# Optimization experiments

Hardware: AMD Instinct MI355X
Metric: run time of the kernel (lower is better)

The kernel has to match this reference:

```python
import jax, jax.numpy as jnp
import numpy as np

N_NODES = 100000
N_EDGES = 1600000
F_IN = 64
HID = 64
N_CLASSES = 45
N_GRAPHS = 256


def gcn_conv(x, src, dst, W, b, n):
    # GCNConv with added self-loops and symmetric normalization (PyG semantics)
    h = x @ W  # [N, H]
    deg = jax.ops.segment_sum(jnp.ones(src.shape[0], h.dtype), dst, num_segments=n) + 1.0
    dinv = jax.lax.rsqrt(deg)  # deg^{-1/2}, deg >= 1 due to self loops
    coef = dinv[src] * dinv[dst]  # [E]
    msg = h[src] * coef[:, None]  # gather + scale
    agg = jax.ops.segment_sum(msg, dst, num_segments=n)  # scatter-add to dst
    agg = agg + h * (dinv * dinv)[:, None]  # self-loop contribution
    return agg + b


def setup_inputs() -> dict:
    key = jax.random.key(0)
    ks = jax.random.split(key, 12)
    x = jax.random.normal(ks[0], (N_NODES, F_IN), dtype=jnp.float32)
    edge_index = jax.random.randint(ks[1], (2, N_EDGES), 0, N_NODES, dtype=jnp.int32)
    batch = jnp.sort(jax.random.randint(ks[2], (N_NODES,), 0, N_GRAPHS, dtype=jnp.int32))
    s1 = 1.0 / np.sqrt(F_IN)
    s2 = 1.0 / np.sqrt(HID)
    W1 = jax.random.uniform(ks[3], (F_IN, HID), jnp.float32, -s1, s1)
    b1 = jnp.zeros((HID,), jnp.float32)
    W2 = jax.random.uniform(ks[4], (HID, HID), jnp.float32, -s2, s2)
    b2 = jnp.zeros((HID,), jnp.float32)
    W3 = jax.random.uniform(ks[5], (HID, HID), jnp.float32, -s2, s2)
    b3 = jnp.zeros((HID,), jnp.float32)
    Wl = jax.random.uniform(ks[6], (HID, N_CLASSES), jnp.float32, -s2, s2)
    bl = jnp.zeros((N_CLASSES,), jnp.float32)
    return {"x": x, "edge_index": edge_index, "batch": batch,
            "W1": W1, "b1": b1, "W2": W2, "b2": b2, "W3": W3, "b3": b3,
            "Wl": Wl, "bl": bl}


def reference(x, edge_index, batch, W1, b1, W2, b2, W3, b3, Wl, bl):
    n = x.shape[0]
    src, dst = edge_index[0], edge_index[1]
    h = jax.nn.relu(gcn_conv(x, src, dst, W1, b1, n))
    h = jax.nn.relu(gcn_conv(h, src, dst, W2, b2, n))
    h = gcn_conv(h, src, dst, W3, b3, n)
    # global mean pool over graph segments
    sums = jax.ops.segment_sum(h, batch, num_segments=N_GRAPHS)  # [G, H]
    cnts = jax.ops.segment_sum(jnp.ones(n, h.dtype), batch, num_segments=N_GRAPHS)
    pooled = sums / jnp.maximum(cnts, 1.0)[:, None]
    # dropout is identity in eval mode
    return pooled @ Wl + bl  # [G, num_classes]
```

## Files before the change

kernel.cpp:

```cpp
#include <hip/hip_runtime.h>
#include <hip/hip_bf16.h>

#define N_NODES   100000
#define N_EDGES   1600000
#define F_IN      64
#define HID       64
#define N_CLASSES 45
#define N_GRAPHS  256
#define SB        392
#define NPB       256
#define CAP       4608
#define WPB       72
#define CHUNK     4096
#define NCHUNK    391
#define NZB       192
#define GEMM_GRID 3125
#define AGGE_GRID 7056
#define NZB2      192
#define ZLEN4_F   1600000
#define ZLEN4_A   1604096

__device__ __forceinline__ float rl_f(float v, int k) {
    return __uint_as_float(__builtin_amdgcn_readlane(__float_as_uint(v), k));
}
__device__ __forceinline__ int rl_i(int v, int k) {
    return __builtin_amdgcn_readlane(v, k);
}
__device__ __forceinline__ unsigned short f2bf(float x) {
    unsigned u = __float_as_uint(x);
    unsigned r = u + 0x7FFFu + ((u >> 16) & 1u);
    return (unsigned short)(r >> 16);
}
__device__ __forceinline__ float bf2f(unsigned short h) {
    return __uint_as_float(((unsigned)h) << 16);
}
__device__ __forceinline__ unsigned scale2(unsigned u, float dv) {
    float lo = __uint_as_float(u << 16) * dv;
    float hi = __uint_as_float(u & 0xFFFF0000u) * dv;
    return (((unsigned)f2bf(hi)) << 16) | (unsigned)f2bf(lo);
}

__global__ __launch_bounds__(256) void k_front(const int* __restrict__ src, const int* __restrict__ dst,
                                               int* __restrict__ bcur, int* __restrict__ binned,
                                               const float* __restrict__ x, const float* __restrict__ W1,
                                               unsigned short* __restrict__ P, float* __restrict__ zbase) {
    int bid = blockIdx.x;
    int t   = threadIdx.x;
    if (bid < NCHUNK) {
        __shared__ int stg[CHUNK];
        __shared__ unsigned short bkt[CHUNK];
        __shared__ int h[512], cur[512], off[512];
        __shared__ int ps[256];
        h[t] = 0; h[t + 256] = 0;
        __syncthreads();
        int base4 = bid * (CHUNK / 4);
        #pragma unroll
        for (int i = 0; i < CHUNK / 1024; i++) {
            int e4 = base4 + i * 256 + t;
            if (e4 < N_EDGES / 4) {
                int4 d = ((const int4*)dst)[e4];
                atomicAdd(&h[d.x >> 8], 1);
                atomicAdd(&h[d.y >> 8], 1);
                atomicAdd(&h[d.z >> 8], 1);
                atomicAdd(&h[d.w >> 8], 1);
            }
        }
        __syncthreads();
        int a0 = h[2 * t], a1 = h[2 * t + 1];
        ps[t] = a0 + a1;
        __syncthreads();
        for (int o = 1; o < 256; o <<= 1) {
            int v = (t >= o) ? ps[t - o] : 0;
            __syncthreads();
            if (t >= o) ps[t] += v;
            __syncthreads();
        }
        int pex = ps[t] - (a0 + a1);
        int e0 = pex, e1 = pex + a0;
        cur[2 * t] = e0; cur[2 * t + 1] = e1;
        if (2 * t < SB && a0 > 0)
            off[2 * t] = (2 * t) * CAP + atomicAdd(&bcur[2 * t], a0) - e0;
        if (2 * t + 1 < SB && a1 > 0)
            off[2 * t + 1] = (2 * t + 1) * CAP + atomicAdd(&bcur[2 * t + 1], a1) - e1;
        __syncthreads();
        int total = ps[255];
        #pragma unroll
        for (int i = 0; i < CHUNK / 1024; i++) {
            int e4 = base4 + i * 256 + t;
            if (e4 < N_EDGES / 4) {
                int4 d  = ((const int4*)dst)[e4];
                int4 s4 = ((const int4*)src)[e4];
                int q;
                q = atomicAdd(&cur[d.x >> 8], 1); stg[q] = s4.x | ((d.x & 255) << 17); bkt[q] = (unsigned short)(d.x >> 8);
                q = atomicAdd(&cur[d.y >> 8], 1); stg[q] = s4.y | ((d.y & 255) << 17); bkt[q] = (unsigned short)(d.y >> 8);
                q = atomicAdd(&cur[d.z >> 8], 1); stg[q] = s4.z | ((d.z & 255) << 17); bkt[q] = (unsigned short)(d.z >> 8);
                q = atomicAdd(&cur[d.w >> 8], 1); stg[q] = s4.w | ((d.w & 255) << 17); bkt[q] = (unsigned short)(d.w >> 8);
            }
        }
        __syncthreads();
        for (int i = t; i < total; i += 256) {
            int b = bkt[i];
            binned[off[b] + i] = stg[i];
        }
    } else if (bid < NCHUNK + NZB) {
        float4 z = make_float4(0.f, 0.f, 0.f, 0.f);
        float4* zp = (float4*)zbase;
        int zb = bid - NCHUNK;
        for (long i = (long)zb * 256 + t; i < (long)ZLEN4_F; i += (long)NZB * 256)
            zp[i] = z;
    } else {
        int gbid = bid - NCHUNK - NZB;
        int lane = t & 63;
        int wv   = t >> 6;
        int base = gbid * 32 + wv * 8;
        float xr[8], acc[8];
        #pragma unroll
        for (int r = 0; r < 8; r++) {
            xr[r]  = x[(size_t)(base + r) * 64 + lane];
            acc[r] = 0.f;
        }
        for (int kb = 0; kb < 64; kb += 8) {
            float wb[8];
            #pragma unroll
            for (int j = 0; j < 8; j++) wb[j] = W1[(kb + j) * 64 + lane];
            #pragma unroll
            for (int j = 0; j < 8; j++) {
                #pragma unroll
                for (int r = 0; r < 8; r++)
                    acc[r] = fmaf(rl_f(xr[r], kb + j), wb[j], acc[r]);
            }
        }
        #pragma unroll
        for (int r = 0; r < 8; r++)
            P[(size_t)(base + r) * 64 + lane] = f2bf(acc[r]);
    }
}

__global__ __launch_bounds__(1024) void k_bcsr(const int* __restrict__ binned, const int* __restrict__ bcur,
                                               float* __restrict__ dinv, float* __restrict__ dinv2,
                                               int* __restrict__ csr, unsigned short* __restrict__ P) {
    __shared__ int bin_s[CAP];
    __shared__ int cs_s[CAP];
    __shared__ int h[NPB];
    __shared__ int ts[NPB];
    __shared__ float sdv[NPB];
    int t = threadIdx.x;
    int b = blockIdx.x;
    int nb0  = b << 8;
    int ebeg = b * CAP;
    int ecnt = bcur[b]; if (ecnt > CAP) ecnt = CAP;
    if (t < NPB) h[t] = 0;
    __syncthreads();
    for (int i = t; i < ecnt; i += 1024) {
        int p = binned[ebeg + i];
        bin_s[i] = p;
        atomicAdd(&h[p >> 17], 1);
    }
    __syncthreads();
    int c = 0;
    if (t < NPB) { c = h[t]; ts[t] = c; }
    __syncthreads();
    for (int o = 1; o < NPB; o <<= 1) {
        int v = (t >= o && t < NPB) ? ts[t - o] : 0;
        __syncthreads();
        if (t >= o && t < NPB) ts[t] += v;
        __syncthreads();
    }
    if (t < NPB) {
        int n = nb0 + t;
        float dval = 0.f;
        if (n < N_NODES) {
            float inv = 1.0f / (float)(c + 1);
            dinv2[n] = inv;
            dval     = sqrtf(inv);
            dinv[n]  = dval;
        }
        sdv[t] = dval;
        h[t] = ts[t] - c;
    }
    __syncthreads();
    for (int i = t; i < ecnt; i += 1024) {
        int p = bin_s[i];
        int q = atomicAdd(&h[p >> 17], 1);
        cs_s[q] = p;
    }
    __syncthreads();
    for (int i = t; i < ecnt; i += 1024)
        csr[ebeg + i] = cs_s[i];
    for (int i = t; i < NPB * 8; i += 1024) {
        int row = i >> 3;
        int nn  = nb0 + row;
        if (nn >= N_NODES) break;
        float dv = sdv[row];
        uint4* pp = (uint4*)P + (size_t)nn * 8 + (i & 7);
        uint4 v = *pp;
        v.x = scale2(v.x, dv); v.y = scale2(v.y, dv);
        v.z = scale2(v.z, dv); v.w = scale2(v.w, dv);
        *pp = v;
    }
}

template<bool POOLI>
__global__ __launch_bounds__(256) void k_gemm(const float* __restrict__ E,
                                              unsigned short* P,
                                              const float* __restrict__ W,
                                              const float* __restrict__ bprev,
                                              const float* __restrict__ bcurr,
                                              const float* __restrict__ dinv,
                                              const float* __restrict__ dinv2,
                                              const int* __restrict__ batch,
                                              float* __restrict__ pool) {
    int lane = threadIdx.x & 63;
    int wv   = threadIdx.x >> 6;
    int base = blockIdx.x * 32 + wv * 8;
    float bp = bprev[lane];
    float xr[8], acc[8], dn[8];
    #pragma unroll
    for (int r = 0; r < 8; r++) dn[r] = dinv[base + r];
    #pragma unroll
    for (int r = 0; r < 8; r++) {
        int n = base + r;
        float hp = bf2f(P[(size_t)n * 64 + lane]);
        float a  = E[(size_t)n * 64 + lane] + fmaf(hp, dn[r], bp);
        xr[r]  = fmaxf(a, 0.f);
        acc[r] = 0.f;
    }
    for (int kb = 0; kb < 64; kb += 8) {
        float wb[8];
        #pragma unroll
        for (int j = 0; j < 8; j++) wb[j] = W[(kb + j) * 64 + lane];
        #pragma unroll
        for (int j = 0; j < 8; j++) {
            #pragma unroll
            for (int r = 0; r < 8; r++)
                acc[r] = fmaf(rl_f(xr[r], kb + j), wb[j], acc[r]);
        }
    }
    #pragma unroll
    for (int r = 0; r < 8; r++)
        P[(size_t)(base + r) * 64 + lane] = f2bf(acc[r] * dn[r]);
    if (POOLI) {
        float bv = bcurr[lane];
        float d2[8];
        #pragma unroll
        for (int r = 0; r < 8; r++) d2[r] = dinv2[base + r];
        int g0 = batch[base], g7 = batch[base + 7];
        if (g0 == g7) {
            float s = 0.f;
            #pragma unroll
            for (int r = 0; r < 8; r++) s += fmaf(acc[r], d2[r], bv);
            atomicAdd(&pool[g0 * 64 + lane], s);
        } else {
            #pragma unroll
            for (int r = 0; r < 8; r++) {
                int g = batch[base + r];
                atomicAdd(&pool[g * 64 + lane], fmaf(acc[r], d2[r], bv));
            }
        }
    }
}

template<bool POOLEP, bool ZROLE>
__global__ __launch_bounds__(256, 8) void k_agge(const unsigned short* __restrict__ Hbuf,
                                                 const int* __restrict__ csr,
                                                 const int* __restrict__ bcur,
                                                 const float* __restrict__ dinv,
                                                 const int* __restrict__ batch,
                                                 float* __restrict__ Out,
                                                 float* __restrict__ zbase) {
    int t = threadIdx.x;
    if (ZROLE && blockIdx.x >= AGGE_GRID) {
        float4 z = make_float4(0.f, 0.f, 0.f, 0.f);
        float4* zp = (float4*)zbase;
        int zb = blockIdx.x - AGGE_GRID;
        for (long i = (long)zb * 256 + t; i < (long)ZLEN4_A; i += (long)NZB2 * 256)
            zp[i] = z;
        return;
    }
    int wv   = t >> 6;
    int lane = t & 63;
    int wid  = blockIdx.x * 4 + wv;
    int b    = wid / WPB;
    int lw   = wid - b * WPB;
    int used = bcur[b]; if (used > CAP) used = CAP;
    int e0   = lw * 64;
    int rem  = used - e0;
    if (rem <= 0) return;
    if (rem > 64) rem = 64;
    int base = b * CAP + e0;

    int p = 0;
    if (lane < rem) p = csr[base + lane];
    int sv = p & 0x1FFFF;
    int dv = p >> 17;

    int dvp = __shfl_up(dv, 1);
    unsigned long long m0 = __ballot(dv != dvp);
    unsigned mlo = __builtin_amdgcn_readfirstlane((unsigned)m0);
    unsigned mhi = __builtin_amdgcn_readfirstlane((unsigned)(m0 >> 32));
    unsigned long long mask = ((((unsigned long long)mhi) << 32) | mlo) & ~1ull;

    auto flush1 = [&](int dl, float a) {
        int dst = (b << 8) + dl;
        if (dst < N_NODES) {
            float val = dinv[dst] * a;
            if (POOLEP) {
                int g = batch[dst];
                atomicAdd(&Out[g * 64 + lane], val);
            } else {
                atomicAdd(&Out[(size_t)dst * 64 + lane], val);
            }
        }
    };

    int cur = rl_i(dv, 0);
    float acc = 0.f;
    int j = 0;
    for (; j + 16 <= rem; j += 16) {
        unsigned short u[16];
        #pragma unroll
        for (int i = 0; i < 16; i++) {
            int s = rl_i(sv, j + i);
            u[i] = Hbuf[(size_t)s * 64 + lane];
        }
        #pragma unroll
        for (int i = 0; i < 16; i++) {
            if ((mask >> (j + i)) & 1) {
                flush1(cur, acc); acc = 0.f; cur = rl_i(dv, j + i);
            }
            acc += bf2f(u[i]);
        }
    }
    for (; j < rem; j++) {
        int s0 = rl_i(sv, j);
        unsigned short u0 = Hbuf[(size_t)s0 * 64 + lane];
        if ((mask >> j) & 1) { flush1(cur, acc); acc = 0.f; cur = rl_i(dv, j); }
        acc += bf2f(u0);
    }
    flush1(cur, acc);
}

__device__ __forceinline__ int lbound(const int* __restrict__ a, int n, int v) {
    int lo = 0, hi = n;
    while (lo < hi) { int m = (lo + hi) >> 1; if (a[m] < v) lo = m + 1; else hi = m; }
    return lo;
}

__global__ __launch_bounds__(64) void k_cls(const float* __restrict__ pool, const int* __restrict__ batch,
                                            const float* __restrict__ Wl, const float* __restrict__ bl,
                                            float* __restrict__ out) {
    __shared__ float pm[64];
    __shared__ int bounds[2];
    int g = blockIdx.x;
    int t = threadIdx.x;
    if (t < 2) bounds[t] = lbound(batch, N_NODES, g + t);
    __syncthreads();
    float cnt = (float)(bounds[1] - bounds[0]);
    pm[t] = pool[g * 64 + t] / fmaxf(cnt, 1.0f);
    __syncthreads();
    if (t < N_CLASSES) {
        float o = bl[t];
        #pragma unroll
        for (int k = 0; k < HID; k++) o = fmaf(pm[k], Wl[k * N_CLASSES + t], o);
        out[g * N_CLASSES + t] = o;
    }
}


extern "C" void kernel_launch(void* const* d_in, const int* in_sizes, int n_in,
                              void* d_out, int out_size, void* d_ws, size_t ws_size,
                              hipStream_t stream) {
    const float* x     = (const float*)d_in[0];
    const int*   eidx  = (const int*)  d_in[1];
    const int*   batch = (const int*)  d_in[2];
    const float* W1 = (const float*)d_in[3];
    const float* b1 = (const float*)d_in[4];
    const float* W2 = (const float*)d_in[5];
    const float* b2 = (const float*)d_in[6];
    const float* W3 = (const float*)d_in[7];
    const float* b3 = (const float*)d_in[8];
    const float* Wl = (const float*)d_in[9];
    const float* bl = (const float*)d_in[10];
    const int* src = eidx;
    const int* dst = eidx + N_EDGES;

    char* p = (char*)d_ws;
    auto alloc = [&](size_t bytes) -> void* {
        void* r = (void*)p;
        p += (bytes + 255) & ~(size_t)255;
        return r;
    };
    float* dinv  = (float*)alloc((size_t)N_NODES * 4);
    float* dinv2 = (float*)alloc((size_t)N_NODES * 4);
    int*   csr   = (int*)  alloc((size_t)SB * CAP * 4);
    unsigned short* P = (unsigned short*)alloc((size_t)N_NODES * 64 * 2);
    float* E1    = (float*)alloc((size_t)N_NODES * 64 * 4);
    float* pool  = (float*)alloc((size_t)N_GRAPHS * 64 * 4);
    float* E2    = (float*)alloc((size_t)N_NODES * 64 * 4);
    int*   bcur  = (int*)  alloc((size_t)SB * 4);
    int*   binned = (int*) alloc((size_t)SB * CAP * 4);

    const int front_grid = NCHUNK + NZB + GEMM_GRID;

    hipMemsetAsync(bcur, 0, (size_t)SB * 4, stream);
    k_front<<<front_grid, 256, 0, stream>>>(src, dst, bcur, binned, x, W1, P, E1);
    k_bcsr <<<SB, 1024, 0, stream>>>(binned, bcur, dinv, dinv2, csr, P);

    k_agge<false, true ><<<AGGE_GRID + NZB2, 256, 0, stream>>>(P, csr, bcur, dinv, batch, E1, pool);
    k_gemm<false><<<GEMM_GRID, 256, 0, stream>>>(E1, P, W2, b1, nullptr, dinv, dinv2, batch, nullptr);
    k_agge<false, false><<<AGGE_GRID, 256, 0, stream>>>(P, csr, bcur, dinv, batch, E2, nullptr);
    k_gemm<true ><<<GEMM_GRID, 256, 0, stream>>>(E2, P, W3, b2, b3, dinv, dinv2, batch, pool);
    k_agge<true , false><<<AGGE_GRID, 256, 0, stream>>>(P, csr, bcur, dinv, batch, pool, nullptr);

    k_cls<<<N_GRAPHS, 64, 0, stream>>>(pool, batch, Wl, bl, (float*)d_out);
}
```

Baseline: 355.3 us.

## Use bf16 MFMA for dense node transforms with pre-transposed bf16 weights

Replaces the per-lane readlane FMA loops in the front GEMM and both k_gemm layers with 16x16x32 bf16 MFMA. Node tiles of 128 rows and the weights are staged in padded shared memory. A small prep kernel converts and transposes W1..W3 to bf16, and the pooling epilogue is reworked around the MFMA output layout with cross-lane shuffles. This cuts scalar FMA and readlane cost in these GEMMs, but rounds inputs and weights to bf16 and adds shared-memory staging plus one extra launch.

```diff
diff --git a/kernel.cpp b/kernel.cpp
--- a/kernel.cpp
+++ b/kernel.cpp
@@ -14,11 +14,16 @@
 #define CHUNK     4096
 #define NCHUNK    391
 #define NZB       192
-#define GEMM_GRID 3125
+#define GEMM_GRID 782
 #define AGGE_GRID 7056
 #define NZB2      192
 #define ZLEN4_F   1600000
 #define ZLEN4_A   1604096
+#define LW        72
+
+typedef __attribute__((ext_vector_type(8))) short bf16x8;
+typedef __attribute__((ext_vector_type(4))) float f32x4;
+union B128 { uint4 u; bf16x8 b; };
 
 __device__ __forceinline__ float rl_f(float v, int k) {
     return __uint_as_float(__builtin_amdgcn_readlane(__float_as_uint(v), k));
@@ -40,9 +45,21 @@
     return (((unsigned)f2bf(hi)) << 16) | (unsigned)f2bf(lo);
 }
 
+__global__ __launch_bounds__(256) void k_prep(const float* __restrict__ W1, const float* __restrict__ W2,
+                                              const float* __restrict__ W3, unsigned short* __restrict__ Wt) {
+    const float* W = (blockIdx.x == 0) ? W1 : (blockIdx.x == 1) ? W2 : W3;
+    unsigned short* o = Wt + blockIdx.x * 4096;
+    int t = threadIdx.x;
+    #pragma unroll
+    for (int i = 0; i < 16; i++) {
+        int e = i * 256 + t;
+        o[e] = f2bf(W[(e & 63) * 64 + (e >> 6)]);
+    }
+}
+
 __global__ __launch_bounds__(256) void k_front(const int* __restrict__ src, const int* __restrict__ dst,
                                                int* __restrict__ bcur, int* __restrict__ binned,
-                                               const float* __restrict__ x, const float* __restrict__ W1,
+                                               const float* __restrict__ x, const unsigned short* __restrict__ Wt1,
                                                unsigned short* __restrict__ P, float* __restrict__ zbase) {
     int bid = blockIdx.x;
     int t   = threadIdx.x;
@@ -109,30 +126,61 @@
         for (long i = (long)zb * 256 + t; i < (long)ZLEN4_F; i += (long)NZB * 256)
             zp[i] = z;
     } else {
-        int gbid = bid - NCHUNK - NZB;
-        int lane = t & 63;
-        int wv   = t >> 6;
-        int base = gbid * 32 + wv * 8;
-        float xr[8], acc[8];
-        #pragma unroll
-        for (int r = 0; r < 8; r++) {
-            xr[r]  = x[(size_t)(base + r) * 64 + lane];
-            acc[r] = 0.f;
-        }
-        for (int kb = 0; kb < 64; kb += 8) {
-            float wb[8];
+        __shared__ unsigned short xin_s[128 * LW];
+        __shared__ unsigned short wt_s[64 * LW];
+        int nb = (bid - NCHUNK - NZB) * 128;
+        #pragma unroll
+        for (int i = 0; i < 16; i++) {
+            int e = i * 256 + t;
+            wt_s[(e >> 6) * LW + (e & 63)] = Wt1[e];
+        }
+        #pragma unroll
+        for (int i = 0; i < 8; i++) {
+            int f = i * 256 + t;
+            int row = f >> 4, q = f & 15;
+            int gR = nb + row;
+            unsigned u0 = 0, u1 = 0;
+            if (gR < N_NODES) {
+                float4 xv = ((const float4*)x)[(size_t)gR * 16 + q];
+                u0 = ((unsigned)f2bf(xv.y) << 16) | f2bf(xv.x);
+                u1 = ((unsigned)f2bf(xv.w) << 16) | f2bf(xv.z);
+            }
+            *(uint2*)&xin_s[row * LW + q * 4] = make_uint2(u0, u1);
+        }
+        __syncthreads();
+        int lane = t & 63, w = t >> 6;
+        int l15 = lane & 15, l4 = lane >> 4;
+        B128 bfr[4][2];
+        #pragma unroll
+        for (int nt = 0; nt < 4; nt++)
             #pragma unroll
-            for (int j = 0; j < 8; j++) wb[j] = W1[(kb + j) * 64 + lane];
+            for (int ks = 0; ks < 2; ks++)
+                bfr[nt][ks].u = *(const uint4*)&wt_s[(nt * 16 + l15) * LW + ks * 32 + l4 * 8];
+        f32x4 acc[2][4] = {};
+        #pragma unroll
+        for (int m = 0; m < 2; m++) {
+            int rb = w * 32 + m * 16;
+            B128 a0, a1;
+            a0.u = *(const uint4*)&xin_s[(rb + l15) * LW +  0 + l4 * 8];
+            a1.u = *(const uint4*)&xin_s[(rb + l15) * LW + 32 + l4 * 8];
             #pragma unroll
-            for (int j = 0; j < 8; j++) {
+            for (int nt = 0; nt < 4; nt++) {
+                acc[m][nt] = __builtin_amdgcn_mfma_f32_16x16x32_bf16(a0.b, bfr[nt][0].b, acc[m][nt], 0, 0, 0);
+                acc[m][nt] = __builtin_amdgcn_mfma_f32_16x16x32_bf16(a1.b, bfr[nt][1].b, acc[m][nt], 0, 0, 0);
+            }
+        }
+        #pragma unroll
+        for (int m = 0; m < 2; m++) {
+            int Rbase = nb + w * 32 + m * 16;
+            #pragma unroll
+            for (int nt = 0; nt < 4; nt++)
                 #pragma unroll
-                for (int r = 0; r < 8; r++)
-                    acc[r] = fmaf(rl_f(xr[r], kb + j), wb[j], acc[r]);
-            }
-        }
-        #pragma unroll
-        for (int r = 0; r < 8; r++)
-            P[(size_t)(base + r) * 64 + lane] = f2bf(acc[r]);
+                for (int r = 0; r < 4; r++) {
+                    int row = Rbase + l4 * 4 + r;
+                    if (row < N_NODES)
+                        P[(size_t)row * 64 + nt * 16 + l15] = f2bf(acc[m][nt][r]);
+                }
+        }
     }
 }
 
@@ -203,58 +251,109 @@
 template<bool POOLI>
 __global__ __launch_bounds__(256) void k_gemm(const float* __restrict__ E,
                                               unsigned short* P,
-                                              const float* __restrict__ W,
+                                              const unsigned short* __restrict__ Wt,
                                               const float* __restrict__ bprev,
                                               const float* __restrict__ bcurr,
                                               const float* __restrict__ dinv,
                                               const float* __restrict__ dinv2,
                                               const int* __restrict__ batch,
                                               float* __restrict__ pool) {
-    int lane = threadIdx.x & 63;
-    int wv   = threadIdx.x >> 6;
-    int base = blockIdx.x * 32 + wv * 8;
-    float bp = bprev[lane];
-    float xr[8], acc[8], dn[8];
+    __shared__ unsigned short xin_s[128 * LW];
+    __shared__ unsigned short wt_s[64 * LW];
+    int t  = threadIdx.x;
+    int nb = blockIdx.x * 128;
     #pragma unroll
-    for (int r = 0; r < 8; r++) dn[r] = dinv[base + r];
+    for (int i = 0; i < 16; i++) {
+        int e = i * 256 + t;
+        wt_s[(e >> 6) * LW + (e & 63)] = Wt[e];
+    }
     #pragma unroll
-    for (int r = 0; r < 8; r++) {
-        int n = base + r;
-        float hp = bf2f(P[(size_t)n * 64 + lane]);
-        float a  = E[(size_t)n * 64 + lane] + fmaf(hp, dn[r], bp);
-        xr[r]  = fmaxf(a, 0.f);
-        acc[r] = 0.f;
-    }
-    for (int kb = 0; kb < 64; kb += 8) {
-        float wb[8];
-        #pragma unroll
-        for (int j = 0; j < 8; j++) wb[j] = W[(kb + j) * 64 + lane];
-        #pragma unroll
-        for (int j = 0; j < 8; j++) {
+    for (int i = 0; i < 8; i++) {
+        int f = i * 256 + t;
+        int row = f >> 4, q = f & 15;
+        int gR = nb + row;
+        unsigned u0 = 0, u1 = 0;
+        if (gR < N_NODES) {
+            float4  ev = ((const float4*)E)[(size_t)gR * 16 + q];
+            ushort4 pv = ((const ushort4*)P)[(size_t)gR * 16 + q];
+            float dn = dinv[gR];
+            float4 bp = ((const float4*)bprev)[q];
+            float x0 = fmaxf(ev.x + fmaf(bf2f(pv.x), dn, bp.x), 0.f);
+            float x1 = fmaxf(ev.y + fmaf(bf2f(pv.y), dn, bp.y), 0.f);
+            float x2 = fmaxf(ev.z + fmaf(bf2f(pv.z), dn, bp.z), 0.f);
+            float x3 = fmaxf(ev.w + fmaf(bf2f(pv.w), dn, bp.w), 0.f);
+            u0 = ((unsigned)f2bf(x1) << 16) | f2bf(x0);
+            u1 = ((unsigned)f2bf(x3) << 16) | f2bf(x2);
+        }
+        *(uint2*)&xin_s[row * LW + q * 4] = make_uint2(u0, u1);
+    }
+    __syncthreads();
+    int lane = t & 63, w = t >> 6;
+    int l15 = lane & 15, l4 = lane >> 4;
+    B128 bfr[4][2];
+    #pragma unroll
+    for (int nt = 0; nt < 4; nt++)
+        #pragma unroll
+        for (int ks = 0; ks < 2; ks++)
+            bfr[nt][ks].u = *(const uint4*)&wt_s[(nt * 16 + l15) * LW + ks * 32 + l4 * 8];
+    f32x4 acc[2][4] = {};
+    #pragma unroll
+    for (int m = 0; m < 2; m++) {
+        int rb = w * 32 + m * 16;
+        B128 a0, a1;
+        a0.u = *(const uint4*)&xin_s[(rb + l15) * LW +  0 + l4 * 8];
+        a1.u = *(const uint4*)&xin_s[(rb + l15) * LW + 32 + l4 * 8];
+        #pragma unroll
+        for (int nt = 0; nt < 4; nt++) {
+            acc[m][nt] = __builtin_amdgcn_mfma_f32_16x16x32_bf16(a0.b, bfr[nt][0].b, acc[m][nt], 0, 0, 0);
+            acc[m][nt] = __builtin_amdgcn_mfma_f32_16x16x32_bf16(a1.b, bfr[nt][1].b, acc[m][nt], 0, 0, 0);
+        }
+    }
+    #pragma unroll
+    for (int m = 0; m < 2; m++) {
+        int Rbase = nb + w * 32 + m * 16;
+        float dnr[4], d2r[4];
+        #pragma unroll
+        for (int r = 0; r < 4; r++) {
+            int row = Rbase + l4 * 4 + r;
+            bool v = row < N_NODES;
+            dnr[r] = v ? dinv[row] : 0.f;
+            d2r[r] = (POOLI && v) ? dinv2[row] : 0.f;
+        }
+        #pragma unroll
+        for (int nt = 0; nt < 4; nt++)
             #pragma unroll
-            for (int r = 0; r < 8; r++)
-                acc[r] = fmaf(rl_f(xr[r], kb + j), wb[j], acc[r]);
-        }
-    }
-    #pragma unroll
-    for (int r = 0; r < 8; r++)
-        P[(size_t)(base + r) * 64 + lane] = f2bf(acc[r] * dn[r]);
-    if (POOLI) {
-        float bv = bcurr[lane];
-        float d2[8];
-        #pragma unroll
-        for (int r = 0; r < 8; r++) d2[r] = dinv2[base + r];
-        int g0 = batch[base], g7 = batch[base + 7];
-        if (g0 == g7) {
-            float s = 0.f;
-            #pragma unroll
-            for (int r = 0; r < 8; r++) s += fmaf(acc[r], d2[r], bv);
-            atomicAdd(&pool[g0 * 64 + lane], s);
-        } else {
-            #pragma unroll
-            for (int r = 0; r < 8; r++) {
-                int g = batch[base + r];
-                atomicAdd(&pool[g * 64 + lane], fmaf(acc[r], d2[r], bv));
+            for (int r = 0; r < 4; r++) {
+                int row = Rbase + l4 * 4 + r;
+                if (row < N_NODES)
+                    P[(size_t)row * 64 + nt * 16 + l15] = f2bf(acc[m][nt][r] * dnr[r]);
+            }
+        if (POOLI) {
+            bool full = (Rbase + 15) < N_NODES;
+            int g0 = -1, g15 = -2;
+            if (full) { g0 = batch[Rbase]; g15 = batch[Rbase + 15]; }
+            if (full && g0 == g15) {
+                #pragma unroll
+                for (int nt = 0; nt < 4; nt++) {
+                    float v = 0.f;
+                    #pragma unroll
+                    for (int r = 0; r < 4; r++) v = fmaf(acc[m][nt][r], d2r[r], v);
+                    v += __shfl_xor(v, 16);
+                    v += __shfl_xor(v, 32);
+                    if (lane < 16)
+                        atomicAdd(&pool[g0 * 64 + nt * 16 + lane], fmaf(16.f, bcurr[nt * 16 + lane], v));
+                }
+            } else if (Rbase < N_NODES) {
+                #pragma unroll
+                for (int nt = 0; nt < 4; nt++) {
+                    float bc = bcurr[nt * 16 + l15];
+                    #pragma unroll
+                    for (int r = 0; r < 4; r++) {
+                        int row = Rbase + l4 * 4 + r;
+                        if (row < N_NODES)
+                            atomicAdd(&pool[batch[row] * 64 + nt * 16 + l15], fmaf(acc[m][nt][r], d2r[r], bc));
+                    }
+                }
             }
         }
     }
@@ -399,17 +498,19 @@
     float* E2    = (float*)alloc((size_t)N_NODES * 64 * 4);
     int*   bcur  = (int*)  alloc((size_t)SB * 4);
     int*   binned = (int*) alloc((size_t)SB * CAP * 4);
+    unsigned short* Wt = (unsigned short*)alloc((size_t)3 * 4096 * 2);
 
     const int front_grid = NCHUNK + NZB + GEMM_GRID;
 
     hipMemsetAsync(bcur, 0, (size_t)SB * 4, stream);
-    k_front<<<front_grid, 256, 0, stream>>>(src, dst, bcur, binned, x, W1, P, E1);
+    k_prep<<<3, 256, 0, stream>>>(W1, W2, W3, Wt);
+    k_front<<<front_grid, 256, 0, stream>>>(src, dst, bcur, binned, x, Wt, P, E1);
     k_bcsr <<<SB, 1024, 0, stream>>>(binned, bcur, dinv, dinv2, csr, P);
 
     k_agge<false, true ><<<AGGE_GRID + NZB2, 256, 0, stream>>>(P, csr, bcur, dinv, batch, E1, pool);
-    k_gemm<false><<<GEMM_GRID, 256, 0, stream>>>(E1, P, W2, b1, nullptr, dinv, dinv2, batch, nullptr);
+    k_gemm<false><<<GEMM_GRID, 256, 0, stream>>>(E1, P, Wt + 4096, b1, nullptr, dinv, dinv2, batch, nullptr);
     k_agge<false, false><<<AGGE_GRID, 256, 0, stream>>>(P, csr, bcur, dinv, batch, E2, nullptr);
-    k_gemm<true ><<<GEMM_GRID, 256, 0, stream>>>(E2, P, W3, b2, b3, dinv, dinv2, batch, pool);
+    k_gemm<true ><<<GEMM_GRID, 256, 0, stream>>>(E2, P, Wt + 8192, b2, b3, dinv, dinv2, batch, pool);
     k_agge<true , false><<<AGGE_GRID, 256, 0, stream>>>(P, csr, bcur, dinv, batch, pool, nullptr);
 
     k_cls<<<N_GRAPHS, 64, 0, stream>>>(pool, batch, Wl, bl, (float*)d_out);
```

Result: faster. 311.6 us (-12.3%).
